# Kernel tuning notes

Measured on AMD Instinct MI355X. Metric: run time of the kernel, lower is better.

Reference implementation:

```python
import jax, jax.numpy as jnp
import numpy as np

EPS = 0.01       # perturbation radius (constructor arg)
MEAN = 0.1307    # MNIST normalize constants from the 'else' branch
SIGMA = 0.3081


def _get_bound(v, eps):
    # torch get_bound detaches eps before taking |.| and summing
    r = jnp.sum(jnp.abs(jax.lax.stop_gradient(eps)), axis=-1)
    return v + r, v - r


def _relu_zono(v, eps):
    # v: [N], eps: [N, E]. Append one fresh (zero) error column, as the torch code does.
    n = v.shape[0]
    eps = jnp.concatenate([eps, jnp.zeros((n, 1), eps.dtype)], axis=-1)  # [N, E+1]
    u, l = _get_bound(v, eps)
    denom = u - l  # = 2*sum|eps| >= 0; guard against 0 for non-crossing rows
    # slopes are created as Parameters = u/(u-l) on the first pass (detached leaf)
    slope = jax.lax.stop_gradient(u / jnp.where(denom == 0, 1.0, denom))
    # at init slope == base = u/(u-l), so the slope <= base branch is taken
    term = (1.0 - slope) * u * 0.5
    crossing = (u > 0) & (l < 0)
    dead = u <= 0
    # torch uses slope.data * values.data for the linear part, + term (term carries grad)
    v_cross = jax.lax.stop_gradient(slope * v) + term
    v_new = jnp.where(dead, 0.0, jnp.where(crossing, v_cross, v))
    eps_cross = jnp.concatenate([slope[:, None] * eps[:, :-1], term[:, None]], axis=-1)
    eps_new = jnp.where(dead[:, None], 0.0, jnp.where(crossing[:, None], eps_cross, eps))
    return v_new, eps_new


def _forward(inputs, W1, b1, W2, b2, W3, b3):
    # initial zonotope build (faithful to source: values = u + l, radii = values - l = u)
    upper = jnp.minimum(inputs + EPS, 1.0)   # upper - relu(upper - 1)
    lower = jnp.maximum(inputs - EPS, 0.0)   # relu(lower)
    values = upper + lower
    eps = jnp.diag((values - lower).flatten())  # [D, D]
    # Normalize layer (the 'else' branch)
    values = (values - MEAN) / SIGMA
    eps = eps / SIGMA
    # Flatten
    v = values.flatten()
    # Linear -> ReLU -> Linear -> ReLU -> Linear
    v = W1 @ v + b1
    eps = W1 @ eps
    v, eps = _relu_zono(v, eps)
    v = W2 @ v + b2
    eps = W2 @ eps
    v, eps = _relu_zono(v, eps)
    v = W3 @ v + b3
    eps = W3 @ eps
    u, l = _get_bound(v, eps)
    return u, l


def setup_inputs() -> dict:
    key = jax.random.key(0)
    ks = jax.random.split(key, 7)
    D, H, O = 1024, 4096, 10
    inputs = jax.random.uniform(ks[0], (1, 1, 32, 32), jnp.float32)
    W1 = jax.random.normal(ks[1], (H, D), jnp.float32) / np.float32(np.sqrt(D))
    b1 = jax.random.normal(ks[2], (H,), jnp.float32) * 0.01
    W2 = jax.random.normal(ks[3], (H, H), jnp.float32) / np.float32(np.sqrt(H))
    b2 = jax.random.normal(ks[4], (H,), jnp.float32) * 0.01
    W3 = jax.random.normal(ks[5], (O, H), jnp.float32) / np.float32(np.sqrt(H))
    b3 = jax.random.normal(ks[6], (O,), jnp.float32) * 0.01
    return {"inputs": inputs, "W1": W1, "b1": b1, "W2": W2, "b2": b2, "W3": W3, "b3": b3}


def reference(inputs, W1, b1, W2, b2, W3, b3):
    return _forward(inputs, W1, b1, W2, b2, W3, b3)
```

## Files before the change

### kernel.cpp

```cpp
#include <hip/hip_runtime.h>
#include <math.h>

#define ZEPS  0.01f
#define ZMEAN 0.1307f
#define ZSIGMA 0.3081f

constexpr int D = 1024, H = 4096, O = 10;

using short8 = __attribute__((ext_vector_type(8))) short;
using f32x4  = __attribute__((ext_vector_type(4))) float;

__device__ inline unsigned short f2bf(float x) {
    unsigned int u = __float_as_uint(x);
    u += 0x7FFFu + ((u >> 16) & 1u);
    return (unsigned short)(u >> 16);
}

__device__ inline void gl_lds16(const void* g, void* l) {
    __builtin_amdgcn_global_load_lds(
        (const __attribute__((address_space(1))) unsigned int*)g,
        (__attribute__((address_space(3))) unsigned int*)l, 16, 0, 0);
}

__device__ inline float zval(float xv) {
    float up = fminf(xv + ZEPS, 1.f);
    float lo = fmaxf(xv - ZEPS, 0.f);
    return (up + lo - ZMEAN) / ZSIGMA;
}
__device__ inline float zdia(float xv) {
    return fminf(xv + ZEPS, 1.f) / ZSIGMA;
}

__device__ inline void relu_params(float v, float r, float& vout, float& aout, float& tout) {
    float u = v + r, l = v - r;
    float denom = u - l;
    float slope = u / (denom == 0.f ? 1.f : denom);
    float term = (1.f - slope) * u * 0.5f;
    bool dead = (u <= 0.f);
    bool crossing = (u > 0.f) && (l < 0.f);
    vout = dead ? 0.f : (crossing ? (slope * v + term) : v);
    aout = dead ? 0.f : (crossing ? slope : 1.f);
    tout = (!dead && crossing) ? term : 0.f;
}

__global__ __launch_bounds__(256) void k_layer1(const float* __restrict__ W1, const float* __restrict__ b1,
                                                const float* __restrict__ x,
                                                float* __restrict__ v1p, float* __restrict__ a1,
                                                float* __restrict__ t1) {
    int i = blockIdx.x, tid = threadIdx.x;
    const float* row = W1 + (size_t)i * D;
    float sv = 0.f, sr = 0.f;
    for (int j = tid; j < D; j += 256) {
        float w = row[j];
        float xv = x[j];
        sv += w * zval(xv);
        sr += fabsf(w) * zdia(xv);
    }
    __shared__ float red1[256], red2[256];
    red1[tid] = sv; red2[tid] = sr;
    __syncthreads();
    for (int off = 128; off; off >>= 1) {
        if (tid < off) { red1[tid] += red1[tid + off]; red2[tid] += red2[tid + off]; }
        __syncthreads();
    }
    if (tid == 0) {
        float v = red1[0] + b1[i];
        relu_params(v, red2[0], v1p[i], a1[i], t1[i]);
    }
}

__global__ __launch_bounds__(256) void k_scaleT(const float* __restrict__ W1, const float* __restrict__ a1,
                                                const float* __restrict__ x,
                                                unsigned short* __restrict__ W1sT) {
    __shared__ float tile[32][33];
    int j0 = blockIdx.x * 32, k0 = blockIdx.y * 32;
    int r = threadIdx.x >> 3;
    int c = (threadIdx.x & 7) * 4;
    float4 w = *(const float4*)&W1[(size_t)(k0 + r) * D + j0 + c];
    float4 xx = *(const float4*)&x[j0 + c];
    float a = a1[k0 + r];
    tile[r][c + 0] = a * w.x * zdia(xx.x);
    tile[r][c + 1] = a * w.y * zdia(xx.y);
    tile[r][c + 2] = a * w.z * zdia(xx.z);
    tile[r][c + 3] = a * w.w * zdia(xx.w);
    __syncthreads();
    ushort4 o;
    o.x = f2bf(tile[c + 0][r]);
    o.y = f2bf(tile[c + 1][r]);
    o.z = f2bf(tile[c + 2][r]);
    o.w = f2bf(tile[c + 3][r]);
    *(ushort4*)&W1sT[(size_t)(j0 + r) * H + k0 + c] = o;
}

__global__ __launch_bounds__(256) void k_v2conv(const float* __restrict__ W2, const float* __restrict__ b2,
                                                const float* __restrict__ v1p, const float* __restrict__ t1,
                                                float* __restrict__ v2, float* __restrict__ t2col,
                                                unsigned short* __restrict__ W2b) {
    int i = blockIdx.x, tid = threadIdx.x;
    const float* row = W2 + (size_t)i * H;
    unsigned short* orow = W2b + (size_t)i * H;
    float sv = 0.f, st = 0.f;
    for (int k0 = tid * 4; k0 < H; k0 += 1024) {
        float4 w = *(const float4*)&row[k0];
        sv += w.x * v1p[k0] + w.y * v1p[k0 + 1] + w.z * v1p[k0 + 2] + w.w * v1p[k0 + 3];
        st += w.x * t1[k0] + w.y * t1[k0 + 1] + w.z * t1[k0 + 2] + w.w * t1[k0 + 3];
        ushort4 o;
        o.x = f2bf(w.x); o.y = f2bf(w.y); o.z = f2bf(w.z); o.w = f2bf(w.w);
        *(ushort4*)&orow[k0] = o;
    }
    __shared__ float red1[256], red2[256];
    red1[tid] = sv; red2[tid] = st;
    __syncthreads();
    for (int off = 128; off; off >>= 1) {
        if (tid < off) { red1[tid] += red1[tid + off]; red2[tid] += red2[tid + off]; }
        __syncthreads();
    }
    if (tid == 0) { v2[i] = red1[0] + b2[i]; t2col[i] = red2[0]; }
}

#define GBK 64
__global__ __launch_bounds__(256) void k_gemm_mfma(const unsigned short* __restrict__ A,
                                                   const unsigned short* __restrict__ B,
                                                   float* __restrict__ C) {
    const int N = D, K = H;
    __shared__ __align__(16) unsigned short As[128 * GBK];
    __shared__ __align__(16) unsigned short Bs[128 * GBK];
    int b = blockIdx.x;
    int u = b & 7, v = b >> 3;
    int z = u >> 2;
    int y = (u & 3) * 8 + (v >> 3);
    int xb = v & 7;
    int tid = threadIdx.x;
    int wave = tid >> 6, lane = tid & 63;
    int bm = y * 128, bn = xb * 128;
    int kbeg = z * (K / 2), kend = kbeg + K / 2;
    float* Cz = C + (size_t)z * ((size_t)H * D);
    int wm = (wave >> 1) * 64, wn = (wave & 1) * 64;

    int sr = lane >> 3;
    int sc = lane & 7;
    int scp = sc ^ sr;
    int r15 = lane & 15, quad = lane >> 4, key = r15 & 7;

    f32x4 acc[4][4];
#pragma unroll
    for (int p = 0; p < 4; ++p)
#pragma unroll
        for (int q = 0; q < 4; ++q) acc[p][q] = (f32x4){0.f, 0.f, 0.f, 0.f};

    for (int k0 = kbeg; k0 < kend; k0 += GBK) {
#pragma unroll
        for (int g = 0; g < 4; ++g) {
            int row = wave * 32 + g * 8;
            gl_lds16(&A[(size_t)(bm + row + sr) * K + k0 + scp * 8], &As[row * GBK]);
            gl_lds16(&B[(size_t)(bn + row + sr) * K + k0 + scp * 8], &Bs[row * GBK]);
        }
        __syncthreads();
#pragma unroll
        for (int kk = 0; kk < 2; ++kk) {
            short8 af[4], bf[4];
#pragma unroll
            for (int mt = 0; mt < 4; ++mt)
                af[mt] = *(const short8*)&As[(wm + mt * 16 + r15) * GBK + (((kk * 4 + quad) ^ key)) * 8];
#pragma unroll
            for (int nt = 0; nt < 4; ++nt)
                bf[nt] = *(const short8*)&Bs[(wn + nt * 16 + r15) * GBK + (((kk * 4 + quad) ^ key)) * 8];
#pragma unroll
            for (int mt = 0; mt < 4; ++mt)
#pragma unroll
                for (int nt = 0; nt < 4; ++nt)
                    acc[mt][nt] = __builtin_amdgcn_mfma_f32_16x16x32_bf16(af[mt], bf[nt], acc[mt][nt], 0, 0, 0);
        }
        __syncthreads();
    }

#pragma unroll
    for (int mt = 0; mt < 4; ++mt) {
        int gr = bm + wm + mt * 16 + quad * 4;
#pragma unroll
        for (int nt = 0; nt < 4; ++nt) {
            int gc = bn + wn + nt * 16 + r15;
            Cz[(size_t)(gr + 0) * N + gc] = acc[mt][nt][0];
            Cz[(size_t)(gr + 1) * N + gc] = acc[mt][nt][1];
            Cz[(size_t)(gr + 2) * N + gc] = acc[mt][nt][2];
            Cz[(size_t)(gr + 3) * N + gc] = acc[mt][nt][3];
        }
    }
}

__global__ __launch_bounds__(256) void k_relu2(const float* __restrict__ e1, const float* __restrict__ e2,
                                               const float* __restrict__ t2col,
                                               const float* __restrict__ v2, const float* __restrict__ W3,
                                               float* __restrict__ v2p,
                                               float* __restrict__ a2, float* __restrict__ t2,
                                               float* __restrict__ w3s) {
    int i = blockIdx.x, tid = threadIdx.x;
    float4 a = ((const float4*)(e1 + (size_t)i * D))[tid];
    float4 b = ((const float4*)(e2 + (size_t)i * D))[tid];
    float s = fabsf(a.x + b.x) + fabsf(a.y + b.y) + fabsf(a.z + b.z) + fabsf(a.w + b.w);
    __shared__ float red[256];
    __shared__ float s_a2;
    red[tid] = s;
    __syncthreads();
    for (int off = 128; off; off >>= 1) {
        if (tid < off) red[tid] += red[tid + off];
        __syncthreads();
    }
    if (tid == 0) {
        float r = red[0] + fabsf(t2col[i]);
        float vo, ao, to;
        relu_params(v2[i], r, vo, ao, to);
        v2p[i] = vo; a2[i] = ao; t2[i] = to;
        s_a2 = ao;
    }
    __syncthreads();
    if (tid < O) w3s[(size_t)i * O + tid] = W3[(size_t)tid * H + i] * s_a2;
}

__global__ __launch_bounds__(256) void k_eps3a(const float* __restrict__ e1, const float* __restrict__ e2,
                                               const float* __restrict__ w3s,
                                               float* __restrict__ pbuf) {
    int jb = blockIdx.x, ib = blockIdx.y;
    int jj = threadIdx.x & 15, s = threadIdx.x >> 4;
    int j = jb * 64 + jj * 4;
    int i0 = ib * 128 + s * 8;
    float acc[4][O];
#pragma unroll
    for (int c = 0; c < 4; ++c)
#pragma unroll
        for (int o = 0; o < O; ++o) acc[c][o] = 0.f;
    for (int ii = 0; ii < 8; ++ii) {
        int i = i0 + ii;
        float4 a = *(const float4*)&e1[(size_t)i * D + j];
        float4 b = *(const float4*)&e2[(size_t)i * D + j];
        float e0 = a.x + b.x, ee1 = a.y + b.y, ee2 = a.z + b.z, ee3 = a.w + b.w;
        const float* w = &w3s[(size_t)i * O];
#pragma unroll
        for (int o = 0; o < O; ++o) {
            float wo = w[o];
            acc[0][o] += wo * e0; acc[1][o] += wo * ee1;
            acc[2][o] += wo * ee2; acc[3][o] += wo * ee3;
        }
    }
    __shared__ float sm[16][64][O];
#pragma unroll
    for (int c = 0; c < 4; ++c)
#pragma unroll
        for (int o = 0; o < O; ++o) sm[s][jj * 4 + c][o] = acc[c][o];
    __syncthreads();
    for (int idx = threadIdx.x; idx < 64 * O; idx += 256) {
        int col = idx / O, o = idx % O;
        float t = 0.f;
#pragma unroll
        for (int ss = 0; ss < 16; ++ss) t += sm[ss][col][o];
        pbuf[((size_t)o * 32 + ib) * D + jb * 64 + col] = t;
    }
}

__global__ __launch_bounds__(256) void k_final(const float* __restrict__ W3, const float* __restrict__ b3,
                                               const float* __restrict__ v2p, const float* __restrict__ a2,
                                               const float* __restrict__ t2col, const float* __restrict__ t2,
                                               const float* __restrict__ pbuf, float* __restrict__ out) {
    int o = blockIdx.x, tid = threadIdx.x;
    float s3 = 0.f;
    for (int j = tid; j < D; j += 256) {
        float t = 0.f;
#pragma unroll
        for (int ib = 0; ib < 32; ++ib) t += pbuf[((size_t)o * 32 + ib) * D + j];
        s3 += fabsf(t);
    }
    const float* row = W3 + (size_t)o * H;
    float sv = 0.f, s1 = 0.f, s2 = 0.f;
    for (int i = tid; i < H; i += 256) {
        float w = row[i];
        sv += w * v2p[i];
        s1 += w * a2[i] * t2col[i];
        s2 += w * t2[i];
    }
    __shared__ float ra[256], rb[256], rc[256], rd[256];
    ra[tid] = sv; rb[tid] = s1; rc[tid] = s2; rd[tid] = s3;
    __syncthreads();
    for (int off = 128; off; off >>= 1) {
        if (tid < off) {
            ra[tid] += ra[tid + off]; rb[tid] += rb[tid + off];
            rc[tid] += rc[tid + off]; rd[tid] += rd[tid + off];
        }
        __syncthreads();
    }
    if (tid == 0) {
        float v3 = ra[0] + b3[o];
        float rr = rd[0] + fabsf(rb[0]) + fabsf(rc[0]);
        out[o] = v3 + rr;
        out[O + o] = v3 - rr;
    }
}

extern "C" void kernel_launch(void* const* d_in, const int* in_sizes, int n_in,
                              void* d_out, int out_size, void* d_ws, size_t ws_size,
                              hipStream_t stream) {
    const float* x  = (const float*)d_in[0];
    const float* W1 = (const float*)d_in[1];
    const float* b1 = (const float*)d_in[2];
    const float* W2 = (const float*)d_in[3];
    const float* b2 = (const float*)d_in[4];
    const float* W3 = (const float*)d_in[5];
    const float* b3 = (const float*)d_in[6];
    float* out = (float*)d_out;

    float* p = (float*)d_ws;
    float* v1p    = p; p += H;
    float* a1     = p; p += H;
    float* t1     = p; p += H;
    float* v2     = p; p += H;
    float* t2col  = p; p += H;
    float* v2p    = p; p += H;
    float* a2     = p; p += H;
    float* t2     = p; p += H;
    float* w3s    = p; p += H * O + 8;
    float* pbuf   = p; p += 32 * O * D;
    float* eps2   = p; p += (size_t)2 * H * D;
    unsigned short* W2b  = (unsigned short*)p;
    unsigned short* W1sT = W2b + (size_t)H * H;
    float* eps2b = eps2 + (size_t)H * D;

    k_layer1<<<H, 256, 0, stream>>>(W1, b1, x, v1p, a1, t1);
    k_scaleT<<<dim3(D / 32, H / 32), 256, 0, stream>>>(W1, a1, x, W1sT);
    k_v2conv<<<H, 256, 0, stream>>>(W2, b2, v1p, t1, v2, t2col, W2b);
    k_gemm_mfma<<<512, 256, 0, stream>>>(W2b, W1sT, eps2);
    k_relu2<<<H, 256, 0, stream>>>(eps2, eps2b, t2col, v2, W3, v2p, a2, t2, w3s);
    k_eps3a<<<dim3(D / 64, 32), 256, 0, stream>>>(eps2, eps2b, w3s, pbuf);
    k_final<<<O, 256, 0, stream>>>(W3, b3, v2p, a2, t2col, t2, pbuf, out);
}
```

Before: 221.6 us.

## Fuse W2 bf16 conversion and layer-2 dot products into the MFMA GEMM

Removes the separate k_v2conv pass. The GEMM now loads fp32 W2 directly, converts it to bf16 in registers with a faster rounding, and stores it swizzled into LDS instead of reading a pre-converted copy. Each block also computes partial W2·v1p and W2·t1 dot products over its K-slice on one of every eight steps, writes them to partial buffers, and k_relu2 reduces them. k_layer1 and k_relu2 switch to one wave per row with shuffle reductions. The cost is that every GEMM block now reads W2 in fp32, doubling the A-operand global traffic, and the synchronous register-path A loads may stall the MFMA loop.

```diff
diff --git a/kernel.cpp b/kernel.cpp
--- a/kernel.cpp
+++ b/kernel.cpp
@@ -14,6 +14,12 @@
     unsigned int u = __float_as_uint(x);
     u += 0x7FFFu + ((u >> 16) & 1u);
     return (unsigned short)(u >> 16);
+}
+
+__device__ inline unsigned int f2bf2_fast(float a, float b) {
+    unsigned int ua = __float_as_uint(a) + 0x8000u;
+    unsigned int ub = __float_as_uint(b) + 0x8000u;
+    return (ua >> 16) | (ub & 0xFFFF0000u);
 }
 
 __device__ inline void gl_lds16(const void* g, void* l) {
@@ -47,25 +53,28 @@
                                                 const float* __restrict__ x,
                                                 float* __restrict__ v1p, float* __restrict__ a1,
                                                 float* __restrict__ t1) {
-    int i = blockIdx.x, tid = threadIdx.x;
+    int wid = threadIdx.x >> 6, lane = threadIdx.x & 63;
+    int i = blockIdx.x * 4 + wid;
     const float* row = W1 + (size_t)i * D;
     float sv = 0.f, sr = 0.f;
-    for (int j = tid; j < D; j += 256) {
-        float w = row[j];
-        float xv = x[j];
-        sv += w * zval(xv);
-        sr += fabsf(w) * zdia(xv);
-    }
-    __shared__ float red1[256], red2[256];
-    red1[tid] = sv; red2[tid] = sr;
-    __syncthreads();
-    for (int off = 128; off; off >>= 1) {
-        if (tid < off) { red1[tid] += red1[tid + off]; red2[tid] += red2[tid + off]; }
-        __syncthreads();
-    }
-    if (tid == 0) {
-        float v = red1[0] + b1[i];
-        relu_params(v, red2[0], v1p[i], a1[i], t1[i]);
+#pragma unroll
+    for (int it = 0; it < 4; ++it) {
+        int j = it * 256 + lane * 4;
+        float4 w = *(const float4*)&row[j];
+        float4 xx = *(const float4*)&x[j];
+        sv += w.x * zval(xx.x) + w.y * zval(xx.y) + w.z * zval(xx.z) + w.w * zval(xx.w);
+        sr += fabsf(w.x) * zdia(xx.x) + fabsf(w.y) * zdia(xx.y) +
+              fabsf(w.z) * zdia(xx.z) + fabsf(w.w) * zdia(xx.w);
+    }
+#pragma unroll
+    for (int m = 1; m <= 32; m <<= 1) {
+        sv += __shfl_xor(sv, m, 64);
+        sr += __shfl_xor(sr, m, 64);
+    }
+    if (lane == 0) {
+        float vo, ao, to;
+        relu_params(sv + b1[i], sr, vo, ao, to);
+        v1p[i] = vo; a1[i] = ao; t1[i] = to;
     }
 }
 
@@ -92,39 +101,18 @@
     *(ushort4*)&W1sT[(size_t)(j0 + r) * H + k0 + c] = o;
 }
 
-__global__ __launch_bounds__(256) void k_v2conv(const float* __restrict__ W2, const float* __restrict__ b2,
-                                                const float* __restrict__ v1p, const float* __restrict__ t1,
-                                                float* __restrict__ v2, float* __restrict__ t2col,
-                                                unsigned short* __restrict__ W2b) {
-    int i = blockIdx.x, tid = threadIdx.x;
-    const float* row = W2 + (size_t)i * H;
-    unsigned short* orow = W2b + (size_t)i * H;
-    float sv = 0.f, st = 0.f;
-    for (int k0 = tid * 4; k0 < H; k0 += 1024) {
-        float4 w = *(const float4*)&row[k0];
-        sv += w.x * v1p[k0] + w.y * v1p[k0 + 1] + w.z * v1p[k0 + 2] + w.w * v1p[k0 + 3];
-        st += w.x * t1[k0] + w.y * t1[k0 + 1] + w.z * t1[k0 + 2] + w.w * t1[k0 + 3];
-        ushort4 o;
-        o.x = f2bf(w.x); o.y = f2bf(w.y); o.z = f2bf(w.z); o.w = f2bf(w.w);
-        *(ushort4*)&orow[k0] = o;
-    }
-    __shared__ float red1[256], red2[256];
-    red1[tid] = sv; red2[tid] = st;
-    __syncthreads();
-    for (int off = 128; off; off >>= 1) {
-        if (tid < off) { red1[tid] += red1[tid + off]; red2[tid] += red2[tid + off]; }
-        __syncthreads();
-    }
-    if (tid == 0) { v2[i] = red1[0] + b2[i]; t2col[i] = red2[0]; }
-}
-
 #define GBK 64
-__global__ __launch_bounds__(256) void k_gemm_mfma(const unsigned short* __restrict__ A,
+__global__ __launch_bounds__(256) void k_gemm_mfma(const float* __restrict__ A,
                                                    const unsigned short* __restrict__ B,
-                                                   float* __restrict__ C) {
+                                                   const float* __restrict__ v1p,
+                                                   const float* __restrict__ t1,
+                                                   float* __restrict__ C,
+                                                   float* __restrict__ vpart,
+                                                   float* __restrict__ tpart) {
     const int N = D, K = H;
     __shared__ __align__(16) unsigned short As[128 * GBK];
     __shared__ __align__(16) unsigned short Bs[128 * GBK];
+    __shared__ float vt[2048], tt[2048];
     int b = blockIdx.x;
     int u = b & 7, v = b >> 3;
     int z = u >> 2;
@@ -133,27 +121,58 @@
     int tid = threadIdx.x;
     int wave = tid >> 6, lane = tid & 63;
     int bm = y * 128, bn = xb * 128;
-    int kbeg = z * (K / 2), kend = kbeg + K / 2;
+    int kbeg = z * (K / 2);
     float* Cz = C + (size_t)z * ((size_t)H * D);
     int wm = (wave >> 1) * 64, wn = (wave & 1) * 64;
 
-    int sr = lane >> 3;
-    int sc = lane & 7;
-    int scp = sc ^ sr;
+    int srow = lane >> 3, sc = lane & 7, scp = sc ^ srow;
     int r15 = lane & 15, quad = lane >> 4, key = r15 & 7;
+    int rowg = tid >> 3, ch = tid & 7;
+    int aswz = ch ^ (rowg & 7);
+
+    for (int idx = tid; idx < 512; idx += 256) {
+        *(float4*)&vt[idx * 4] = *(const float4*)&v1p[kbeg + idx * 4];
+        *(float4*)&tt[idx * 4] = *(const float4*)&t1[kbeg + idx * 4];
+    }
+    __syncthreads();
 
     f32x4 acc[4][4];
 #pragma unroll
     for (int p = 0; p < 4; ++p)
 #pragma unroll
         for (int q = 0; q < 4; ++q) acc[p][q] = (f32x4){0.f, 0.f, 0.f, 0.f};
-
-    for (int k0 = kbeg; k0 < kend; k0 += GBK) {
+    float sv[4] = {0.f, 0.f, 0.f, 0.f}, st[4] = {0.f, 0.f, 0.f, 0.f};
+
+    for (int s = 0; s < (K / 2) / GBK; ++s) {
+        int k0 = kbeg + s * GBK;
 #pragma unroll
         for (int g = 0; g < 4; ++g) {
             int row = wave * 32 + g * 8;
-            gl_lds16(&A[(size_t)(bm + row + sr) * K + k0 + scp * 8], &As[row * GBK]);
-            gl_lds16(&B[(size_t)(bn + row + sr) * K + k0 + scp * 8], &Bs[row * GBK]);
+            gl_lds16(&B[(size_t)(bn + row + srow) * K + k0 + scp * 8], &Bs[row * GBK]);
+        }
+        bool dodot = ((s & 7) == xb);
+#pragma unroll
+        for (int g = 0; g < 4; ++g) {
+            int row = g * 32 + rowg;
+            const float* ap = &A[(size_t)(bm + row) * K + k0 + ch * 8];
+            float4 a0 = *(const float4*)ap;
+            float4 a1v = *(const float4*)(ap + 4);
+            if (dodot) {
+                const float* vp = &vt[s * 64 + ch * 8];
+                const float* tp = &tt[s * 64 + ch * 8];
+                float4 v0 = *(const float4*)vp, v1 = *(const float4*)(vp + 4);
+                float4 t0 = *(const float4*)tp, t1v = *(const float4*)(tp + 4);
+                sv[g] += a0.x * v0.x + a0.y * v0.y + a0.z * v0.z + a0.w * v0.w
+                       + a1v.x * v1.x + a1v.y * v1.y + a1v.z * v1.z + a1v.w * v1.w;
+                st[g] += a0.x * t0.x + a0.y * t0.y + a0.z * t0.z + a0.w * t0.w
+                       + a1v.x * t1v.x + a1v.y * t1v.y + a1v.z * t1v.z + a1v.w * t1v.w;
+            }
+            uint4 hh;
+            hh.x = f2bf2_fast(a0.x, a0.y);
+            hh.y = f2bf2_fast(a0.z, a0.w);
+            hh.z = f2bf2_fast(a1v.x, a1v.y);
+            hh.w = f2bf2_fast(a1v.z, a1v.w);
+            *(uint4*)&As[row * GBK + aswz * 8] = hh;
         }
         __syncthreads();
 #pragma unroll
@@ -186,35 +205,48 @@
             Cz[(size_t)(gr + 3) * N + gc] = acc[mt][nt][3];
         }
     }
+
+#pragma unroll
+    for (int g = 0; g < 4; ++g) {
+        float a = sv[g], bb = st[g];
+        a += __shfl_xor(a, 1, 64); a += __shfl_xor(a, 2, 64); a += __shfl_xor(a, 4, 64);
+        bb += __shfl_xor(bb, 1, 64); bb += __shfl_xor(bb, 2, 64); bb += __shfl_xor(bb, 4, 64);
+        if (ch == 0) {
+            int i = bm + g * 32 + rowg;
+            vpart[(size_t)(z * 8 + xb) * H + i] = a;
+            tpart[(size_t)(z * 8 + xb) * H + i] = bb;
+        }
+    }
 }
 
 __global__ __launch_bounds__(256) void k_relu2(const float* __restrict__ e1, const float* __restrict__ e2,
-                                               const float* __restrict__ t2col,
-                                               const float* __restrict__ v2, const float* __restrict__ W3,
-                                               float* __restrict__ v2p,
-                                               float* __restrict__ a2, float* __restrict__ t2,
+                                               const float* __restrict__ vpart, const float* __restrict__ tpart,
+                                               const float* __restrict__ b2, const float* __restrict__ W3,
+                                               float* __restrict__ v2p, float* __restrict__ a2,
+                                               float* __restrict__ t2, float* __restrict__ t2col,
                                                float* __restrict__ w3s) {
-    int i = blockIdx.x, tid = threadIdx.x;
-    float4 a = ((const float4*)(e1 + (size_t)i * D))[tid];
-    float4 b = ((const float4*)(e2 + (size_t)i * D))[tid];
-    float s = fabsf(a.x + b.x) + fabsf(a.y + b.y) + fabsf(a.z + b.z) + fabsf(a.w + b.w);
-    __shared__ float red[256];
-    __shared__ float s_a2;
-    red[tid] = s;
-    __syncthreads();
-    for (int off = 128; off; off >>= 1) {
-        if (tid < off) red[tid] += red[tid + off];
-        __syncthreads();
-    }
-    if (tid == 0) {
-        float r = red[0] + fabsf(t2col[i]);
-        float vo, ao, to;
-        relu_params(v2[i], r, vo, ao, to);
-        v2p[i] = vo; a2[i] = ao; t2[i] = to;
-        s_a2 = ao;
-    }
-    __syncthreads();
-    if (tid < O) w3s[(size_t)i * O + tid] = W3[(size_t)tid * H + i] * s_a2;
+    int wid = threadIdx.x >> 6, lane = threadIdx.x & 63;
+    int i = blockIdx.x * 4 + wid;
+    float s = 0.f;
+#pragma unroll
+    for (int it = 0; it < 4; ++it) {
+        int j = it * 256 + lane * 4;
+        float4 a = *(const float4*)&e1[(size_t)i * D + j];
+        float4 b = *(const float4*)&e2[(size_t)i * D + j];
+        s += fabsf(a.x + b.x) + fabsf(a.y + b.y) + fabsf(a.z + b.z) + fabsf(a.w + b.w);
+    }
+    float ve = (lane < 16) ? vpart[(size_t)lane * H + i] : 0.f;
+    float te = (lane < 16) ? tpart[(size_t)lane * H + i] : 0.f;
+#pragma unroll
+    for (int m = 1; m <= 32; m <<= 1) {
+        s += __shfl_xor(s, m, 64);
+        ve += __shfl_xor(ve, m, 64);
+        te += __shfl_xor(te, m, 64);
+    }
+    float vo, ao, to;
+    relu_params(ve + b2[i], s + fabsf(te), vo, ao, to);
+    if (lane == 0) { v2p[i] = vo; a2[i] = ao; t2[i] = to; t2col[i] = te; }
+    if (lane < O) w3s[(size_t)i * O + lane] = W3[(size_t)lane * H + i] * ao;
 }
 
 __global__ __launch_bounds__(256) void k_eps3a(const float* __restrict__ e1, const float* __restrict__ e2,
@@ -311,23 +343,22 @@
     float* v1p    = p; p += H;
     float* a1     = p; p += H;
     float* t1     = p; p += H;
-    float* v2     = p; p += H;
     float* t2col  = p; p += H;
     float* v2p    = p; p += H;
     float* a2     = p; p += H;
     float* t2     = p; p += H;
     float* w3s    = p; p += H * O + 8;
+    float* vpart  = p; p += 16 * H;
+    float* tpart  = p; p += 16 * H;
     float* pbuf   = p; p += 32 * O * D;
     float* eps2   = p; p += (size_t)2 * H * D;
-    unsigned short* W2b  = (unsigned short*)p;
-    unsigned short* W1sT = W2b + (size_t)H * H;
+    unsigned short* W1sT = (unsigned short*)p;
     float* eps2b = eps2 + (size_t)H * D;
 
-    k_layer1<<<H, 256, 0, stream>>>(W1, b1, x, v1p, a1, t1);
+    k_layer1<<<H / 4, 256, 0, stream>>>(W1, b1, x, v1p, a1, t1);
     k_scaleT<<<dim3(D / 32, H / 32), 256, 0, stream>>>(W1, a1, x, W1sT);
-    k_v2conv<<<H, 256, 0, stream>>>(W2, b2, v1p, t1, v2, t2col, W2b);
-    k_gemm_mfma<<<512, 256, 0, stream>>>(W2b, W1sT, eps2);
-    k_relu2<<<H, 256, 0, stream>>>(eps2, eps2b, t2col, v2, W3, v2p, a2, t2, w3s);
+    k_gemm_mfma<<<512, 256, 0, stream>>>(W2, W1sT, v1p, t1, eps2, vpart, tpart);
+    k_relu2<<<H / 4, 256, 0, stream>>>(eps2, eps2b, vpart, tpart, b2, W3, v2p, a2, t2, t2col, w3s);
     k_eps3a<<<dim3(D / 64, 32), 256, 0, stream>>>(eps2, eps2b, w3s, pbuf);
     k_final<<<O, 256, 0, stream>>>(W3, b3, v2p, a2, t2col, t2, pbuf, out);
 }
```

Result: slower. 230.1 us (+3.8%).
